# Optimization experiments

Hardware: AMD Instinct MI355X
Metric: run time of the kernel (lower is better)

The kernel has to match this reference:

```python
import jax, jax.numpy as jnp
import numpy as np

B, S, D, H, DC, HC, M = 2, 2048, 1024, 16, 64, 16, 4096
DH = D // H  # head_dim = 64


def _ln(x, g, b, eps=1e-5):
    m = jnp.mean(x, axis=-1, keepdims=True)
    v = jnp.var(x, axis=-1, keepdims=True)
    return (x - m) * jax.lax.rsqrt(v + eps) * g + b


def setup_inputs() -> dict:
    key = jax.random.key(0)
    ks = jax.random.split(key, 10)
    def w(k, shape, fan_in):
        return jax.random.normal(k, shape, jnp.float32) * (fan_in ** -0.5)
    return {
        "h": jax.random.normal(ks[0], (B, S, D), jnp.float32),
        "z": jax.random.normal(ks[1], (B, S, DC), jnp.float32),
        # Linear weights stored [in, out] (transpose of torch layout)
        "wv": w(ks[2], (D, D), D),   "bv": jnp.zeros((D,), jnp.float32),
        "wca": w(ks[3], (DC, H * HC), DC), "bca": jnp.zeros((H * HC,), jnp.float32),
        "wcn": w(ks[4], (D, DC), D), "bcn": jnp.zeros((DC,), jnp.float32),
        "wo": w(ks[5], (D, D), D),   "bo": jnp.zeros((D,), jnp.float32),
        "gamma": jnp.zeros((1, H, 1, 1), jnp.float32),
        "w1": w(ks[6], (D, M), D),   "b1": jnp.zeros((M,), jnp.float32),
        "w2": w(ks[7], (M, D), M),   "b2": jnp.zeros((D,), jnp.float32),
        "ln1_g": jnp.ones((D,), jnp.float32),  "ln1_b": jnp.zeros((D,), jnp.float32),
        "ln2_g": jnp.ones((D,), jnp.float32),  "ln2_b": jnp.zeros((D,), jnp.float32),
        "lnc_g": jnp.ones((DC,), jnp.float32), "lnc_b": jnp.zeros((DC,), jnp.float32),
    }


def reference(h, z, wv, bv, wca, bca, wcn, bcn, wo, bo, gamma,
              w1, b1, w2, b2, ln1_g, ln1_b, ln2_g, ln2_b, lnc_g, lnc_b):
    hn = _ln(h, ln1_g, ln1_b)
    # values: [B,S,H,DH]
    value = (hn @ wv + bv).reshape(B, S, H, DH)
    # per-head coordinates: [B,S,H,HC]
    zh = (z @ wca + bca).reshape(B, S, H, HC)
    # pairwise squared distances per head: ||zq||^2 + ||zk||^2 - 2 zq.zk
    z_sq = jnp.sum(zh * zh, axis=-1).transpose(0, 2, 1)        # [B,H,S]
    dot = jnp.einsum('bqhc,bkhc->bhqk', zh, zh)                # [B,H,S,S]
    sq_dist = jnp.maximum(z_sq[:, :, :, None] + z_sq[:, :, None, :] - 2.0 * dot, 0.0)
    g = jax.nn.softplus(gamma)                                 # [1,H,1,1]
    attn = jax.nn.softmax(-g * sq_dist, axis=-1)               # [B,H,S,S]
    attn_out = jnp.einsum('bhqk,bkhd->bqhd', attn, value).reshape(B, S, D)
    h_attn = attn_out @ wo + bo
    z_next = hn @ wcn + bcn
    h = h + h_attn
    # FFN (dropout is identity in eval); torch GELU default is exact (erf)
    hn2 = _ln(h, ln2_g, ln2_b)
    ffn = jax.nn.gelu(hn2 @ w1 + b1, approximate=False) @ w2 + b2
    h = h + ffn
    z_out = _ln(z + z_next, lnc_g, lnc_b)
    return h, z_out
```

## Files before the change

kernel.cpp:

```cpp
#include <hip/hip_runtime.h>

#define USH unsigned short

__device__ __forceinline__ float b2f(USH u) {
    union { unsigned int i; float f; } x; x.i = ((unsigned int)u) << 16; return x.f;
}
__device__ __forceinline__ USH f2b(float f) {
    union { float f; unsigned int i; } x; x.f = f;
    unsigned int r = x.i + (0x7fffu + ((x.i >> 16) & 1u));
    return (USH)(r >> 16);
}
__device__ __forceinline__ float ldf(const USH* p)  { return b2f(*p); }
__device__ __forceinline__ float ldf(const float* p){ return *p; }
__device__ __forceinline__ void stf(USH* p, float v)  { *p = f2b(v); }
__device__ __forceinline__ void stf(float* p, float v){ *p = v; }

#define GLOAD16(gp, lp) __builtin_amdgcn_global_load_lds(                     \
    (const __attribute__((address_space(1))) void*)(gp),                      \
    (__attribute__((address_space(3))) void*)(lp), 16, 0, 0)

typedef __attribute__((ext_vector_type(8))) __bf16 bf16x8;
typedef __attribute__((ext_vector_type(4))) float  floatx4;

__global__ __launch_bounds__(256) void transpose_f2b(const float* __restrict__ W,
                                                     USH* __restrict__ WT,
                                                     int K, int N) {
    __shared__ USH t[64][72];
    int n0 = blockIdx.x * 64, k0 = blockIdx.y * 64;
    int tid = threadIdx.x;
    int kr = tid >> 4, nc = (tid & 15) * 4;
#pragma unroll
    for (int r = 0; r < 4; r++) {
        int k = kr + r * 16;
        float4 v = *(const float4*)(W + (size_t)(k0 + k) * N + n0 + nc);
        t[nc + 0][k] = f2b(v.x); t[nc + 1][k] = f2b(v.y);
        t[nc + 2][k] = f2b(v.z); t[nc + 3][k] = f2b(v.w);
    }
    __syncthreads();
    int nr = tid >> 2, kc = (tid & 3) * 8;
#pragma unroll
    for (int r = 0; r < 2; r++) {
        int k = kc + r * 32;
        *(int4*)(WT + (size_t)(n0 + nr) * K + k0 + k) = *(const int4*)&t[nr][k];
    }
}

template <typename TX>
__global__ __launch_bounds__(256) void ln_rows(const TX* __restrict__ x,
                                               const float* __restrict__ g,
                                               const float* __restrict__ bb,
                                               USH* __restrict__ y) {
    int row = blockIdx.x, tid = threadIdx.x;
    const TX* xr = x + (size_t)row * 1024 + tid * 4;
    float v[4];
#pragma unroll
    for (int i = 0; i < 4; i++) v[i] = ldf(xr + i);
    float s  = v[0] + v[1] + v[2] + v[3];
    float ss = v[0]*v[0] + v[1]*v[1] + v[2]*v[2] + v[3]*v[3];
#pragma unroll
    for (int o = 32; o; o >>= 1) { s += __shfl_down(s, o); ss += __shfl_down(ss, o); }
    __shared__ float red[10];
    int w = tid >> 6;
    if ((tid & 63) == 0) { red[w] = s; red[4 + w] = ss; }
    __syncthreads();
    if (tid == 0) {
        float S = red[0] + red[1] + red[2] + red[3];
        float SS = red[4] + red[5] + red[6] + red[7];
        float mean = S * (1.f / 1024.f);
        float var  = SS * (1.f / 1024.f) - mean * mean;
        red[8] = mean; red[9] = rsqrtf(var + 1e-5f);
    }
    __syncthreads();
    float mean = red[8], rstd = red[9];
    USH* yr = y + (size_t)row * 1024 + tid * 4;
#pragma unroll
    for (int i = 0; i < 4; i++) {
        int c = tid * 4 + i;
        yr[i] = f2b((v[i] - mean) * rstd * g[c] + bb[c]);
    }
}

__global__ __launch_bounds__(256) void zh_kernel(const float* __restrict__ z,
                                                 const float* __restrict__ wca,
                                                 const float* __restrict__ bca,
                                                 const float* __restrict__ gamma,
                                                 USH* __restrict__ zq_pack,
                                                 USH* __restrict__ zk_pack) {
    int row = blockIdx.x, n = threadIdx.x;
    __shared__ float zrow[64];
    if (n < 64) zrow[n] = z[(size_t)row * 64 + n];
    __syncthreads();
    float s = bca[n];
#pragma unroll 8
    for (int k = 0; k < 64; k++) s = fmaf(zrow[k], wca[(size_t)k * 256 + n], s);
    int h = n >> 4, c = n & 15;
    float gvl = log1pf(__expf(gamma[h])) * 1.44269504f;
    USH u = f2b(s);
    float sv = b2f(u);
    float sq = sv * sv;
    sq += __shfl_xor(sq, 1); sq += __shfl_xor(sq, 2);
    sq += __shfl_xor(sq, 4); sq += __shfl_xor(sq, 8);
    size_t base = ((size_t)h * 4096 + row) * 32;
    zk_pack[base + c] = u;
    zq_pack[base + c] = f2b(2.f * gvl * s);
    if (c == 0) {
        USH hi = f2b(sq);
        float lo = sq - b2f(hi);
        unsigned int kw0 = 0x3F80u | ((unsigned int)hi << 16);
        unsigned int kw1 = (unsigned int)f2b(lo);
        uint4 kv = {kw0, kw1, 0u, 0u};
        uint4 zz = {0u, 0u, 0u, 0u};
        *(uint4*)(zk_pack + base + 16) = kv;
        *(uint4*)(zk_pack + base + 24) = zz;
        unsigned int qw0 = (unsigned int)f2b(-gvl * sq) | ((unsigned int)f2b(-gvl) << 16);
        unsigned int qw1 = (unsigned int)f2b(-gvl);
        uint4 qv = {qw0, qw1, 0u, 0u};
        *(uint4*)(zq_pack + base + 16) = qv;
        *(uint4*)(zq_pack + base + 24) = zz;
    }
}

template <int EPI, int MI, int NI, typename TRES, typename TOUT>
__global__ __launch_bounds__(256) void gemm_kernel(const USH* __restrict__ A,
                                                   const USH* __restrict__ WT,
                                                   const float* __restrict__ bias,
                                                   const TRES* __restrict__ res,
                                                   TOUT* __restrict__ out,
                                                   int M, int N, int K) {
    constexpr int BM = MI * 32;
    constexpr int BN = NI * 32;
    __shared__ __align__(16) USH lA[BM][64];
    __shared__ __align__(16) USH lB[BN][64];
    int tid = threadIdx.x;
    int lane = tid & 63, wave = tid >> 6;
    int wr = wave >> 1, wc = wave & 1;
    int quad = lane >> 4, l15 = lane & 15;
    int m0 = blockIdx.x * BM, n0 = blockIdx.y * BN;

    int srow = tid >> 3;
    int k8   = tid & 7;
    int scol = (k8 ^ (srow & 7)) * 8;

    const USH* gA = A + (size_t)(m0 + srow) * K + scol;
    const USH* gB = WT + (size_t)(n0 + srow) * K + scol;
    USH* lA0 = &lA[0][0] + tid * 8;
    USH* lB0 = &lB[0][0] + tid * 8;
    int xo = (l15 & 7) * 8;

    floatx4 acc[MI][NI] = {};

    for (int k0 = 0; k0 < K; k0 += 64) {
#pragma unroll
        for (int c = 0; c < MI; c++)
            GLOAD16(gA + (size_t)c * 32 * K + k0, lA0 + c * 2048);
#pragma unroll
        for (int c = 0; c < NI; c++)
            GLOAD16(gB + (size_t)c * 32 * K + k0, lB0 + c * 2048);
        __syncthreads();

#pragma unroll
        for (int ks = 0; ks < 2; ks++) {
            bf16x8 bfr[NI];
#pragma unroll
            for (int ni = 0; ni < NI; ni++)
                bfr[ni] = *(const bf16x8*)&lB[wc * (NI * 16) + ni * 16 + l15][(ks * 32 + quad * 8) ^ xo];
#pragma unroll
            for (int mi = 0; mi < MI; mi++) {
                bf16x8 afr = *(const bf16x8*)&lA[wr * (MI * 16) + mi * 16 + l15][(ks * 32 + quad * 8) ^ xo];
#pragma unroll
                for (int ni = 0; ni < NI; ni++)
                    acc[mi][ni] = __builtin_amdgcn_mfma_f32_16x16x32_bf16(afr, bfr[ni], acc[mi][ni], 0, 0, 0);
            }
        }
        __syncthreads();
    }

    float bias_v[NI];
#pragma unroll
    for (int ni = 0; ni < NI; ni++) bias_v[ni] = bias[n0 + wc * (NI * 16) + ni * 16 + l15];

#pragma unroll
    for (int mi = 0; mi < MI; mi++) {
#pragma unroll
        for (int r = 0; r < 4; r++) {
            int row = m0 + wr * (MI * 16) + mi * 16 + quad * 4 + r;
            size_t base = (size_t)row * N;
#pragma unroll
            for (int ni = 0; ni < NI; ni++) {
                int col = n0 + wc * (NI * 16) + ni * 16 + l15;
                float v = acc[mi][ni][r] + bias_v[ni];
                if (EPI == 2) {
                    float t = v * v;
                    float a = fmaf(t, -0.0713548162726f, -1.59576912161f);
                    v = v * __builtin_amdgcn_rcpf(1.f + __expf(v * a));
                }
                if (EPI == 1 || EPI == 3) v += ldf(res + base + col);
                stf(out + base + col, v);
            }
        }
    }
}

__global__ __launch_bounds__(512) void attn8_kernel(const USH* __restrict__ zq_pack,
                                                    const USH* __restrict__ zk_pack,
                                                    const USH* __restrict__ value,
                                                    USH* __restrict__ attn_out) {
    int b = blockIdx.x >> 4, h = blockIdx.x & 15;
    int q0 = blockIdx.y * 128;
    int tid = threadIdx.x, lane = tid & 63, wq = tid >> 6;
    int quad = lane >> 4, l15 = lane & 15;

    __shared__ __align__(16) USH Qb[128][40];
    __shared__ __align__(16) USH KbT[64][40];
    __shared__ __align__(16) USH VbT[64][72];
    __shared__ __align__(16) USH Pb[8][16][72];

    const size_t zrow0 = (size_t)b * 2048;
    const USH* zq = zq_pack + ((size_t)h * 4096 + zrow0) * 32;
    const USH* zk = zk_pack + ((size_t)h * 4096 + zrow0) * 32;
    const size_t vbase = zrow0 * 1024 + h * 64;

    {
        int row = tid >> 2, c0 = (tid & 3) * 8;
        *(uint4*)&Qb[row][c0] = *(const uint4*)(zq + (size_t)(q0 + row) * 32 + c0);
    }
    __syncthreads();

    bf16x8 afragQ = *(const bf16x8*)&Qb[wq * 16 + l15][quad * 8];

    union { unsigned int u[4]; bf16x8 v; } onesu;
#pragma unroll
    for (int i = 0; i < 4; i++) onesu.u[i] = 0x3F803F80u;
    bf16x8 ones = onesu.v;

    floatx4 oacc[4] = {};
    floatx4 lacc = {};

    int key2 = (tid & 31) * 2;
    int dh0  = (tid >> 5) * 8;
    int krow = (tid - 256) >> 2, kc0 = ((tid - 256) & 3) * 8;
    int4 vta, vtb; uint4 kreg;

    if (tid < 256) {
        const USH* s0 = value + vbase + (size_t)key2 * 1024 + dh0;
        vta = *(const int4*)s0;
        vtb = *(const int4*)(s0 + 1024);
    } else {
        kreg = *(const uint4*)(zk + (size_t)krow * 32 + kc0);
    }

    for (int kt = 0; kt < 2048; kt += 64) {
        __syncthreads();
        if (tid < 256) {
            const USH* ua = (const USH*)&vta;
            const USH* ub = (const USH*)&vtb;
#pragma unroll
            for (int e = 0; e < 8; e++) {
                unsigned int dw = (unsigned int)ua[e] | ((unsigned int)ub[e] << 16);
                *(unsigned int*)&VbT[dh0 + e][key2] = dw;
            }
            if (kt + 64 < 2048) {
                const USH* s0 = value + vbase + (size_t)(kt + 64 + key2) * 1024 + dh0;
                vta = *(const int4*)s0;
                vtb = *(const int4*)(s0 + 1024);
            }
        } else {
            *(uint4*)&KbT[krow][kc0] = kreg;
            if (kt + 64 < 2048)
                kreg = *(const uint4*)(zk + (size_t)(kt + 64 + krow) * 32 + kc0);
        }
        __syncthreads();

        bf16x8 bk[4];
#pragma unroll
        for (int ni = 0; ni < 4; ni++)
            bk[ni] = *(const bf16x8*)&KbT[ni * 16 + l15][quad * 8];

        floatx4 sacc[4];
#pragma unroll
        for (int ni = 0; ni < 4; ni++) {
            floatx4 zz = {};
            sacc[ni] = __builtin_amdgcn_mfma_f32_16x16x32_bf16(afragQ, bk[ni], zz, 0, 0, 0);
        }
#pragma unroll
        for (int r = 0; r < 4; r++) {
#pragma unroll
            for (int ni = 0; ni < 4; ni++) {
                float pf = exp2f(sacc[ni][r]);
                union { float f; unsigned int i; } cv; cv.f = pf;
                Pb[wq][quad * 4 + r][ni * 16 + l15] = (USH)(cv.i >> 16);
            }
        }

#pragma unroll
        for (int ks2 = 0; ks2 < 2; ks2++) {
            bf16x8 bv[4];
#pragma unroll
            for (int nd = 0; nd < 4; nd++)
                bv[nd] = *(const bf16x8*)&VbT[nd * 16 + l15][ks2 * 32 + quad * 8];
            bf16x8 ap = *(const bf16x8*)&Pb[wq][l15][ks2 * 32 + quad * 8];
#pragma unroll
            for (int nd = 0; nd < 4; nd++)
                oacc[nd] = __builtin_amdgcn_mfma_f32_16x16x32_bf16(ap, bv[nd], oacc[nd], 0, 0, 0);
            lacc = __builtin_amdgcn_mfma_f32_16x16x32_bf16(ap, ones, lacc, 0, 0, 0);
        }
    }

#pragma unroll
    for (int r = 0; r < 4; r++) {
        float inv = 1.f / lacc[r];
        int row = q0 + wq * 16 + quad * 4 + r;
        USH* o = attn_out + (zrow0 + row) * 1024 + h * 64;
#pragma unroll
        for (int nd = 0; nd < 4; nd++) o[nd * 16 + l15] = f2b(oacc[nd][r] * inv);
    }
}

__global__ __launch_bounds__(64) void lnc_kernel(const float* __restrict__ z,
                                                 const float* __restrict__ zn,
                                                 const float* __restrict__ g,
                                                 const float* __restrict__ bb,
                                                 float* __restrict__ out) {
    int row = blockIdx.x, t = threadIdx.x;
    float v = z[(size_t)row * 64 + t] + zn[(size_t)row * 64 + t];
    float s = v, ss = v * v;
#pragma unroll
    for (int o = 32; o; o >>= 1) { s += __shfl_xor(s, o); ss += __shfl_xor(ss, o); }
    float mean = s * (1.f / 64.f);
    float rstd = rsqrtf(ss * (1.f / 64.f) - mean * mean + 1e-5f);
    out[(size_t)row * 64 + t] = (v - mean) * rstd * g[t] + bb[t];
}

extern "C" void kernel_launch(void* const* d_in, const int* in_sizes, int n_in,
                              void* d_out, int out_size, void* d_ws, size_t ws_size,
                              hipStream_t stream) {
    char* p = (char*)d_ws;
    USH*   value   = (USH*)(p);
    USH*   attn_o  = (USH*)(p + ((size_t)8  << 20));
    USH*   wcnT    = (USH*)(p + ((size_t)8  << 20));
    USH*   zq_pack = (USH*)(p + ((size_t)16 << 20));
    USH*   zk_pack = (USH*)(p + ((size_t)20 << 20));
    USH*   hn      = (USH*)(p + ((size_t)24 << 20));
    USH*   mid     = (USH*)(p);
    USH*   hn2     = (USH*)(p + ((size_t)32 << 20));
    float* znext   = (float*)(p + ((size_t)40 << 20));
    USH*   wvT     = (USH*)(p + ((size_t)41 << 20));
    USH*   woT     = (USH*)(p + ((size_t)43 << 20));
    USH*   w1T     = (USH*)(p + ((size_t)45 << 20));
    USH*   w2T     = (USH*)(p + ((size_t)53 << 20));

    const float *h    = (const float*)d_in[0],  *z    = (const float*)d_in[1];
    const float *wv   = (const float*)d_in[2],  *bv   = (const float*)d_in[3];
    const float *wca  = (const float*)d_in[4],  *bca  = (const float*)d_in[5];
    const float *wcn  = (const float*)d_in[6],  *bcn  = (const float*)d_in[7];
    const float *wo   = (const float*)d_in[8],  *bo   = (const float*)d_in[9];
    const float *gam  = (const float*)d_in[10];
    const float *w1   = (const float*)d_in[11], *b1   = (const float*)d_in[12];
    const float *w2   = (const float*)d_in[13], *b2   = (const float*)d_in[14];
    const float *ln1g = (const float*)d_in[15], *ln1b = (const float*)d_in[16];
    const float *ln2g = (const float*)d_in[17], *ln2b = (const float*)d_in[18];
    const float *lncg = (const float*)d_in[19], *lncb = (const float*)d_in[20];

    float* out_h = (float*)d_out;
    float* out_z = out_h + (size_t)4096 * 1024;
    float* h1    = out_h;

    transpose_f2b<<<dim3(16, 16), 256, 0, stream>>>(wv, wvT, 1024, 1024);
    transpose_f2b<<<dim3(16, 16), 256, 0, stream>>>(wo, woT, 1024, 1024);
    transpose_f2b<<<dim3(64, 16), 256, 0, stream>>>(w1, w1T, 1024, 4096);
    transpose_f2b<<<dim3(16, 64), 256, 0, stream>>>(w2, w2T, 4096, 1024);
    transpose_f2b<<<dim3(1, 16),  256, 0, stream>>>(wcn, wcnT, 1024, 64);

    ln_rows<float><<<4096, 256, 0, stream>>>(h, ln1g, ln1b, hn);
    zh_kernel<<<4096, 256, 0, stream>>>(z, wca, bca, gam, zq_pack, zk_pack);
    gemm_kernel<0, 4, 2, USH, USH><<<dim3(32, 16), 256, 0, stream>>>(hn, wvT, bv, (const USH*)nullptr, value, 4096, 1024, 1024);
    gemm_kernel<0, 1, 1, float, float><<<dim3(128, 2), 256, 0, stream>>>(hn, wcnT, bcn, (const float*)nullptr, znext, 4096, 64, 1024);
    attn8_kernel<<<dim3(32, 16), 512, 0, stream>>>(zq_pack, zk_pack, value, attn_o);
    gemm_kernel<1, 4, 2, float, float><<<dim3(32, 16), 256, 0, stream>>>(attn_o, woT, bo, h, h1, 4096, 1024, 1024);
    ln_rows<float><<<4096, 256, 0, stream>>>(h1, ln2g, ln2b, hn2);
    gemm_kernel<2, 4, 4, USH, USH><<<dim3(32, 32), 256, 0, stream>>>(hn2, w1T, b1, (const USH*)nullptr, mid, 4096, 4096, 1024);
    gemm_kernel<3, 4, 2, float, float><<<dim3(32, 16), 256, 0, stream>>>(mid, w2T, b2, h1, out_h, 4096, 1024, 4096);
    lnc_kernel<<<4096, 64, 0, stream>>>(z, znext, lncg, lncb, out_z);
}
```

Measured before the change: 380.5 us.

## Load attention keys straight to registers and parametrize GEMM K-tile depth

```diff
diff --git a/kernel.cpp b/kernel.cpp
--- a/kernel.cpp
+++ b/kernel.cpp
@@ -120,26 +120,30 @@
     }
 }
 
-template <int EPI, int MI, int NI, typename TRES, typename TOUT>
+template <int EPI, int MI, int NI, int KB, typename TRES, typename TOUT>
 __global__ __launch_bounds__(256) void gemm_kernel(const USH* __restrict__ A,
                                                    const USH* __restrict__ WT,
                                                    const float* __restrict__ bias,
                                                    const TRES* __restrict__ res,
                                                    TOUT* __restrict__ out,
                                                    int M, int N, int K) {
-    constexpr int BM = MI * 32;
-    constexpr int BN = NI * 32;
-    __shared__ __align__(16) USH lA[BM][64];
-    __shared__ __align__(16) USH lB[BN][64];
+    constexpr int BM  = MI * 32;
+    constexpr int BN  = NI * 32;
+    constexpr int GR  = KB / 8;
+    constexpr int RPC = 2048 / KB;
+    constexpr int ACH = BM / RPC;
+    constexpr int BCH = BN / RPC;
+    __shared__ __align__(16) USH lA[BM][KB];
+    __shared__ __align__(16) USH lB[BN][KB];
     int tid = threadIdx.x;
     int lane = tid & 63, wave = tid >> 6;
     int wr = wave >> 1, wc = wave & 1;
     int quad = lane >> 4, l15 = lane & 15;
     int m0 = blockIdx.x * BM, n0 = blockIdx.y * BN;
 
-    int srow = tid >> 3;
-    int k8   = tid & 7;
-    int scol = (k8 ^ (srow & 7)) * 8;
+    int srow = tid / GR;
+    int kg   = tid % GR;
+    int scol = (kg ^ (srow & 7)) * 8;
 
     const USH* gA = A + (size_t)(m0 + srow) * K + scol;
     const USH* gB = WT + (size_t)(n0 + srow) * K + scol;
@@ -149,17 +153,17 @@
 
     floatx4 acc[MI][NI] = {};
 
-    for (int k0 = 0; k0 < K; k0 += 64) {
-#pragma unroll
-        for (int c = 0; c < MI; c++)
-            GLOAD16(gA + (size_t)c * 32 * K + k0, lA0 + c * 2048);
-#pragma unroll
-        for (int c = 0; c < NI; c++)
-            GLOAD16(gB + (size_t)c * 32 * K + k0, lB0 + c * 2048);
+    for (int k0 = 0; k0 < K; k0 += KB) {
+#pragma unroll
+        for (int c = 0; c < ACH; c++)
+            GLOAD16(gA + (size_t)c * RPC * K + k0, lA0 + c * 2048);
+#pragma unroll
+        for (int c = 0; c < BCH; c++)
+            GLOAD16(gB + (size_t)c * RPC * K + k0, lB0 + c * 2048);
         __syncthreads();
 
 #pragma unroll
-        for (int ks = 0; ks < 2; ks++) {
+        for (int ks = 0; ks < KB / 32; ks++) {
             bf16x8 bfr[NI];
 #pragma unroll
             for (int ni = 0; ni < NI; ni++)
@@ -201,7 +205,7 @@
     }
 }
 
-__global__ __launch_bounds__(512) void attn8_kernel(const USH* __restrict__ zq_pack,
+__global__ __launch_bounds__(512) void attn9_kernel(const USH* __restrict__ zq_pack,
                                                     const USH* __restrict__ zk_pack,
                                                     const USH* __restrict__ value,
                                                     USH* __restrict__ attn_out) {
@@ -211,7 +215,6 @@
     int quad = lane >> 4, l15 = lane & 15;
 
     __shared__ __align__(16) USH Qb[128][40];
-    __shared__ __align__(16) USH KbT[64][40];
     __shared__ __align__(16) USH VbT[64][72];
     __shared__ __align__(16) USH Pb[8][16][72];
 
@@ -237,51 +240,50 @@
     floatx4 lacc = {};
 
     int key2 = (tid & 31) * 2;
-    int dh0  = (tid >> 5) * 8;
-    int krow = (tid - 256) >> 2, kc0 = ((tid - 256) & 3) * 8;
-    int4 vta, vtb; uint4 kreg;
-
-    if (tid < 256) {
+    int dh0  = (tid >> 5) * 4;
+    int2 vta, vtb;
+
+    bf16x8 bk0[4], bk1[4];
+#define LOADBK(dst, ktv) do {                                                  \
+        int kk_ = (ktv) < 2048 ? (ktv) : 0;                                    \
+        _Pragma("unroll")                                                      \
+        for (int ni_ = 0; ni_ < 4; ni_++)                                      \
+            dst[ni_] = *(const bf16x8*)(zk + (size_t)(kk_ + ni_ * 16 + l15) * 32 + quad * 8); \
+    } while (0)
+
+    {
         const USH* s0 = value + vbase + (size_t)key2 * 1024 + dh0;
-        vta = *(const int4*)s0;
-        vtb = *(const int4*)(s0 + 1024);
-    } else {
-        kreg = *(const uint4*)(zk + (size_t)krow * 32 + kc0);
-    }
-
-    for (int kt = 0; kt < 2048; kt += 64) {
+        vta = *(const int2*)s0;
+        vtb = *(const int2*)(s0 + 1024);
+    }
+    LOADBK(bk0, 0);
+
+    auto body = [&](int kt, bf16x8 (&bkc)[4], bf16x8 (&bkn)[4]) {
         __syncthreads();
-        if (tid < 256) {
+        {
             const USH* ua = (const USH*)&vta;
             const USH* ub = (const USH*)&vtb;
 #pragma unroll
-            for (int e = 0; e < 8; e++) {
+            for (int e = 0; e < 4; e++) {
                 unsigned int dw = (unsigned int)ua[e] | ((unsigned int)ub[e] << 16);
                 *(unsigned int*)&VbT[dh0 + e][key2] = dw;
             }
             if (kt + 64 < 2048) {
                 const USH* s0 = value + vbase + (size_t)(kt + 64 + key2) * 1024 + dh0;
-                vta = *(const int4*)s0;
-                vtb = *(const int4*)(s0 + 1024);
-            }
-        } else {
-            *(uint4*)&KbT[krow][kc0] = kreg;
-            if (kt + 64 < 2048)
-                kreg = *(const uint4*)(zk + (size_t)(kt + 64 + krow) * 32 + kc0);
+                vta = *(const int2*)s0;
+                vtb = *(const int2*)(s0 + 1024);
+            }
         }
         __syncthreads();
-
-        bf16x8 bk[4];
-#pragma unroll
-        for (int ni = 0; ni < 4; ni++)
-            bk[ni] = *(const bf16x8*)&KbT[ni * 16 + l15][quad * 8];
 
         floatx4 sacc[4];
 #pragma unroll
         for (int ni = 0; ni < 4; ni++) {
             floatx4 zz = {};
-            sacc[ni] = __builtin_amdgcn_mfma_f32_16x16x32_bf16(afragQ, bk[ni], zz, 0, 0, 0);
-        }
+            sacc[ni] = __builtin_amdgcn_mfma_f32_16x16x32_bf16(afragQ, bkc[ni], zz, 0, 0, 0);
+        }
+        LOADBK(bkn, kt + 64);
+
 #pragma unroll
         for (int r = 0; r < 4; r++) {
 #pragma unroll
@@ -304,7 +306,13 @@
                 oacc[nd] = __builtin_amdgcn_mfma_f32_16x16x32_bf16(ap, bv[nd], oacc[nd], 0, 0, 0);
             lacc = __builtin_amdgcn_mfma_f32_16x16x32_bf16(ap, ones, lacc, 0, 0, 0);
         }
-    }
+    };
+
+    for (int kt = 0; kt < 2048; kt += 128) {
+        body(kt, bk0, bk1);
+        body(kt + 64, bk1, bk0);
+    }
+#undef LOADBK
 
 #pragma unroll
     for (int r = 0; r < 4; r++) {
@@ -373,12 +381,12 @@
 
     ln_rows<float><<<4096, 256, 0, stream>>>(h, ln1g, ln1b, hn);
     zh_kernel<<<4096, 256, 0, stream>>>(z, wca, bca, gam, zq_pack, zk_pack);
-    gemm_kernel<0, 4, 2, USH, USH><<<dim3(32, 16), 256, 0, stream>>>(hn, wvT, bv, (const USH*)nullptr, value, 4096, 1024, 1024);
-    gemm_kernel<0, 1, 1, float, float><<<dim3(128, 2), 256, 0, stream>>>(hn, wcnT, bcn, (const float*)nullptr, znext, 4096, 64, 1024);
-    attn8_kernel<<<dim3(32, 16), 512, 0, stream>>>(zq_pack, zk_pack, value, attn_o);
-    gemm_kernel<1, 4, 2, float, float><<<dim3(32, 16), 256, 0, stream>>>(attn_o, woT, bo, h, h1, 4096, 1024, 1024);
+    gemm_kernel<0, 4, 2, 128, USH, USH><<<dim3(32, 16), 256, 0, stream>>>(hn, wvT, bv, (const USH*)nullptr, value, 4096, 1024, 1024);
+    gemm_kernel<0, 1, 1, 64, float, float><<<dim3(128, 2), 256, 0, stream>>>(hn, wcnT, bcn, (const float*)nullptr, znext, 4096, 64, 1024);
+    attn9_kernel<<<dim3(32, 16), 512, 0, stream>>>(zq_pack, zk_pack, value, attn_o);
+    gemm_kernel<1, 4, 2, 128, float, float><<<dim3(32, 16), 256, 0, stream>>>(attn_o, woT, bo, h, h1, 4096, 1024, 1024);
     ln_rows<float><<<4096, 256, 0, stream>>>(h1, ln2g, ln2b, hn2);
-    gemm_kernel<2, 4, 4, USH, USH><<<dim3(32, 32), 256, 0, stream>>>(hn2, w1T, b1, (const USH*)nullptr, mid, 4096, 4096, 1024);
-    gemm_kernel<3, 4, 2, float, float><<<dim3(32, 16), 256, 0, stream>>>(mid, w2T, b2, h1, out_h, 4096, 1024, 4096);
+    gemm_kernel<2, 4, 4, 64, USH, USH><<<dim3(32, 32), 256, 0, stream>>>(hn2, w1T, b1, (const USH*)nullptr, mid, 4096, 4096, 1024);
+    gemm_kernel<3, 4, 2, 128, float, float><<<dim3(32, 16), 256, 0, stream>>>(mid, w2T, b2, h1, out_h, 4096, 1024, 4096);
     lnc_kernel<<<4096, 64, 0, stream>>>(z, znext, lncg, lncb, out_z);
 }
```

Result: faster. 366.2 us (-3.7%).
